# Optimization experiments

Measured on AMD Instinct MI355X. Metric: run time of the kernel, lower is better.

The kernel has to match this reference:

```python
import jax, jax.numpy as jnp
import numpy as np

N_NODES = 100000
N_EDGES = 3200000
F_IN = 16
H1 = 50
H2 = 20


def gcn_conv(x, W, b, src, dst, ew, n):
    """GCNConv with add_self_loops=True and symmetric normalization."""
    xw = x @ W  # [n, out]  (transform first: out < in traffic)
    loop = jnp.arange(n, dtype=src.dtype)
    src_f = jnp.concatenate([src, loop])
    dst_f = jnp.concatenate([dst, loop])
    ew_f = jnp.concatenate([ew, jnp.ones((n,), ew.dtype)])
    deg = jax.ops.segment_sum(ew_f, dst_f, num_segments=n)
    dinv = jnp.where(deg > 0, jax.lax.rsqrt(deg), 0.0)
    norm = dinv[src_f] * ew_f * dinv[dst_f]  # [E+n]
    agg = jax.ops.segment_sum(norm[:, None] * xw[src_f], dst_f, num_segments=n)
    return agg + b


def tgcn_cell(x, H, src, dst, ew, n, p):
    # p: dict of params for one TGCN cell
    cz = gcn_conv(x, p['wz'], p['bz'], src, dst, ew, n)
    Z = jax.nn.sigmoid(jnp.concatenate([cz, H], axis=1) @ p['lz_w'].T + p['lz_b'])
    cr = gcn_conv(x, p['wr'], p['br'], src, dst, ew, n)
    R = jax.nn.sigmoid(jnp.concatenate([cr, H], axis=1) @ p['lr_w'].T + p['lr_b'])
    ch = gcn_conv(x, p['wh'], p['bh'], src, dst, ew, n)
    Ht = jnp.tanh(jnp.concatenate([ch, H * R], axis=1) @ p['lh_w'].T + p['lh_b'])
    return Z * H + (1.0 - Z) * Ht


def _cell_params(key, fin, fout):
    ks = jax.random.split(key, 6)
    s_c = 1.0 / np.sqrt(fin)
    s_l = 1.0 / np.sqrt(2 * fout)
    names = ['z', 'r', 'h']
    p = {}
    for i, nm in enumerate(names):
        p['w' + nm] = jax.random.normal(ks[2 * i], (fin, fout), jnp.float32) * s_c
        p['b' + nm] = jnp.zeros((fout,), jnp.float32)
        p['l' + nm + '_w'] = jax.random.normal(ks[2 * i + 1], (fout, 2 * fout), jnp.float32) * s_l
        p['l' + nm + '_b'] = jnp.zeros((fout,), jnp.float32)
    return p


def setup_inputs() -> dict:
    key = jax.random.key(0)
    k = jax.random.split(key, 6)
    x = jax.random.normal(k[0], (N_NODES, F_IN), jnp.float32)
    edge_index = jax.random.randint(k[1], (2, N_EDGES), 0, N_NODES, jnp.int32)
    edge_weight = jax.random.uniform(k[2], (N_EDGES,), jnp.float32)
    p1 = _cell_params(k[3], F_IN, H1)
    p2 = _cell_params(k[4], H1, H2)
    inp = {'x': x, 'edge_index': edge_index, 'edge_weight': edge_weight}
    for nm, v in p1.items():
        inp['c1_' + nm] = v
    for nm, v in p2.items():
        inp['c2_' + nm] = v
    inp['lin_w'] = jax.random.normal(k[5], (1, H2), jnp.float32) * (1.0 / np.sqrt(H2))
    inp['lin_b'] = jnp.zeros((1,), jnp.float32)
    return inp


def reference(x, edge_index, edge_weight,
              c1_wz, c1_bz, c1_lz_w, c1_lz_b, c1_wr, c1_br, c1_lr_w, c1_lr_b,
              c1_wh, c1_bh, c1_lh_w, c1_lh_b,
              c2_wz, c2_bz, c2_lz_w, c2_lz_b, c2_wr, c2_br, c2_lr_w, c2_lr_b,
              c2_wh, c2_bh, c2_lh_w, c2_lh_b,
              lin_w, lin_b):
    n = x.shape[0]
    src, dst = edge_index[0], edge_index[1]
    p1 = dict(wz=c1_wz, bz=c1_bz, lz_w=c1_lz_w, lz_b=c1_lz_b,
              wr=c1_wr, br=c1_br, lr_w=c1_lr_w, lr_b=c1_lr_b,
              wh=c1_wh, bh=c1_bh, lh_w=c1_lh_w, lh_b=c1_lh_b)
    p2 = dict(wz=c2_wz, bz=c2_bz, lz_w=c2_lz_w, lz_b=c2_lz_b,
              wr=c2_wr, br=c2_br, lr_w=c2_lr_w, lr_b=c2_lr_b,
              wh=c2_wh, bh=c2_bh, lh_w=c2_lh_w, lh_b=c2_lh_b)
    h = tgcn_cell(x, jnp.zeros((n, H1), x.dtype), src, dst, edge_weight, n, p1)
    h = jax.nn.relu(h)  # dropout is identity in eval mode
    h = tgcn_cell(h, jnp.zeros((n, H2), x.dtype), src, dst, edge_weight, n, p2)
    h = jax.nn.relu(h)
    return h @ lin_w.T + lin_b  # [n, 1]
```

## Files before the change

### kernel.cpp

```cpp
#include <hip/hip_runtime.h>
#include <math.h>

#define N_NODES 100000
#define N_EDGES 3200000
#define F_IN 16
#define H1 50
#define H2 20
#define C1 100
#define C2 40
#define STRIDE 72
#define NB 391
#define BCAP 9216
#define EPT_A 16

__global__ void k_binA(const int* __restrict__ dst, const int* __restrict__ src,
                       const float* __restrict__ ew, int* __restrict__ gcur,
                       int2* __restrict__ ebuf) {
    __shared__ int cnt[NB];
    __shared__ int base[NB];
    int tid = threadIdx.x;
    for (int b = tid; b < NB; b += 256) cnt[b] = 0;
    __syncthreads();
    int e0 = blockIdx.x * (256 * EPT_A);
    unsigned meta[EPT_A], ewb[EPT_A];
    int bb[EPT_A], rr[EPT_A];
#pragma unroll
    for (int i = 0; i < EPT_A; ++i) {
        int e = e0 + i * 256 + tid;
        bool v = (e < N_EDGES);
        int d = v ? dst[e] : 0;
        int s = v ? src[e] : 0;
        float w = v ? ew[e] : 0.f;
        int b = d >> 8;
        int r = 0;
        if (v) r = atomicAdd(&cnt[b], 1);
        meta[i] = (unsigned)s | ((unsigned)(d & 255) << 17);
        ewb[i]  = __float_as_uint(w);
        bb[i]   = v ? b : -1;
        rr[i]   = r;
    }
    __syncthreads();
    for (int b = tid; b < NB; b += 256) {
        int c = cnt[b];
        base[b] = c ? atomicAdd(&gcur[b], c) : 0;
    }
    __syncthreads();
#pragma unroll
    for (int i = 0; i < EPT_A; ++i) {
        if (bb[i] >= 0) {
            int p = base[bb[i]] + rr[i];
            if (p < BCAP)
                ebuf[(size_t)bb[i] * BCAP + p] = make_int2((int)meta[i], (int)ewb[i]);
        }
    }
}

__global__ void k_binB(const int* __restrict__ gcur, const int2* __restrict__ ebuf,
                       int* __restrict__ cur, float* __restrict__ dinv,
                       int2* __restrict__ se) {
    __shared__ int   lcur[256];
    __shared__ float ldeg[256];
    int tid = threadIdx.x;
    int b   = blockIdx.x;
    if (tid < 256) { lcur[tid] = 0; ldeg[tid] = 0.f; }
    __syncthreads();
    int nE = min(gcur[b], BCAP);
    const int2* eb = ebuf + (size_t)b * BCAP;
    for (int i = tid; i < nE; i += 512) {
        int2 rec = eb[i];
        unsigned m = (unsigned)rec.x;
        int dlow = (int)(m >> 17);
        int s    = (int)(m & 0x1FFFFu);
        int r = atomicAdd(&lcur[dlow], 1);
        int node = (b << 8) + dlow;
        if (r < STRIDE)
            se[(size_t)node * STRIDE + r] = make_int2(s, rec.y);
        atomicAdd(&ldeg[dlow], __uint_as_float((unsigned)rec.y));
    }
    __syncthreads();
    if (tid < 256) {
        int node = (b << 8) + tid;
        if (node < N_NODES) {
            cur[node]  = node * STRIDE + min(lcur[tid], STRIDE);
            dinv[node] = rsqrtf(ldeg[tid] + 1.0f);
        }
    }
}

__global__ void k_y(const float* __restrict__ x, const float* __restrict__ dinv,
                    float* __restrict__ y) {
    int t = blockIdx.x * blockDim.x + threadIdx.x;
    int i = t >> 3, j = t & 7;
    if (i >= N_NODES) return;
    float2 v = ((const float2*)x)[(unsigned)i * 8 + j];
    float di = dinv[i];
    v.x *= di; v.y *= di;
    ((float2*)y)[(unsigned)i * 8 + j] = v;
}

__global__ void k_gather1(const int* __restrict__ cur, const int2* __restrict__ se,
                          const float* __restrict__ y, float* __restrict__ g) {
    int t = blockIdx.x * blockDim.x + threadIdx.x;
    int node = t >> 3, j = t & 7;
    if (node >= N_NODES) return;
    int beg = node * STRIDE;
    int end = min(cur[node], beg + STRIDE);
    const float2* y2 = (const float2*)y;
    float2 a0 = {0.f, 0.f}, a1 = {0.f, 0.f}, a2 = {0.f, 0.f}, a3 = {0.f, 0.f};
    int k = beg;
    for (; k + 4 <= end; k += 4) {
        int2 p0 = se[k], p1 = se[k + 1], p2 = se[k + 2], p3 = se[k + 3];
        float2 v0 = y2[(unsigned)p0.x * 8 + j];
        float2 v1 = y2[(unsigned)p1.x * 8 + j];
        float2 v2 = y2[(unsigned)p2.x * 8 + j];
        float2 v3 = y2[(unsigned)p3.x * 8 + j];
        float w0 = __int_as_float(p0.y), w1 = __int_as_float(p1.y);
        float w2 = __int_as_float(p2.y), w3 = __int_as_float(p3.y);
        a0.x = fmaf(w0, v0.x, a0.x); a0.y = fmaf(w0, v0.y, a0.y);
        a1.x = fmaf(w1, v1.x, a1.x); a1.y = fmaf(w1, v1.y, a1.y);
        a2.x = fmaf(w2, v2.x, a2.x); a2.y = fmaf(w2, v2.y, a2.y);
        a3.x = fmaf(w3, v3.x, a3.x); a3.y = fmaf(w3, v3.y, a3.y);
    }
    for (; k < end; ++k) {
        int2 p = se[k];
        float2 v = y2[(unsigned)p.x * 8 + j];
        float w = __int_as_float(p.y);
        a0.x = fmaf(w, v.x, a0.x); a0.y = fmaf(w, v.y, a0.y);
    }
    float2 r;
    r.x = (a0.x + a1.x) + (a2.x + a3.x);
    r.y = (a0.y + a1.y) + (a2.y + a3.y);
    ((float2*)g)[(unsigned)node * 8 + j] = r;
}

__global__ __launch_bounds__(256) void k_conv1_gate_xs2(
        const float* __restrict__ g, const float* __restrict__ x,
        const float* __restrict__ dinv,
        const float* __restrict__ wz, const float* __restrict__ wh,
        const float* __restrict__ cbz, const float* __restrict__ cbh,
        const float* __restrict__ lzw, const float* __restrict__ lzb,
        const float* __restrict__ lhw, const float* __restrict__ lhb,
        const float* __restrict__ w2z, const float* __restrict__ w2h,
        float* __restrict__ xs2) {
    int i = blockIdx.x * blockDim.x + threadIdx.x;
    if (i >= N_NODES) return;
    float di = dinv[i];

    float tv[F_IN];
    const float4* g4 = (const float4*)(g + (size_t)i * F_IN);
    const float4* x4 = (const float4*)(x + (size_t)i * F_IN);
#pragma unroll
    for (int q = 0; q < F_IN / 4; ++q) {
        float4 gv = g4[q], xv = x4[q];
        tv[4 * q + 0] = fmaf(di, xv.x, gv.x);
        tv[4 * q + 1] = fmaf(di, xv.y, gv.y);
        tv[4 * q + 2] = fmaf(di, xv.z, gv.z);
        tv[4 * q + 3] = fmaf(di, xv.w, gv.w);
    }

    float cz[H1], ch[H1];
#pragma unroll
    for (int j = 0; j < H1; ++j) {
        float az = 0.f, ah = 0.f;
#pragma unroll
        for (int k = 0; k < F_IN; ++k) {
            az = fmaf(tv[k], wz[k * H1 + j], az);
            ah = fmaf(tv[k], wh[k * H1 + j], ah);
        }
        cz[j] = fmaf(di, az, cbz[j]);
        ch[j] = fmaf(di, ah, cbh[j]);
    }

    float acc[C2];
#pragma unroll
    for (int c = 0; c < C2; ++c) acc[c] = 0.f;
    for (int j = 0; j < H1; ++j) {
        const float* zr = lzw + j * (2 * H1);
        const float* hrw = lhw + j * (2 * H1);
        float az = lzb[j], ah = lhb[j];
#pragma unroll
        for (int k = 0; k < H1; ++k) {
            az = fmaf(cz[k], zr[k], az);
            ah = fmaf(ch[k], hrw[k], ah);
        }
        float Z   = 1.f / (1.f + __expf(-az));
        float Ht  = 1.f - 2.f / (__expf(2.f * ah) + 1.f);
        float hrj = fmaxf((1.f - Z) * Ht, 0.f);
        const float* w2zr = w2z + j * H2;
        const float* w2hr = w2h + j * H2;
#pragma unroll
        for (int c = 0; c < H2; ++c) {
            acc[c]      = fmaf(hrj, w2zr[c], acc[c]);
            acc[H2 + c] = fmaf(hrj, w2hr[c], acc[H2 + c]);
        }
    }
    float4* o4 = (float4*)(xs2 + (size_t)i * C2);
#pragma unroll
    for (int q = 0; q < C2 / 4; ++q) {
        float4 v;
        v.x = di * acc[4 * q + 0]; v.y = di * acc[4 * q + 1];
        v.z = di * acc[4 * q + 2]; v.w = di * acc[4 * q + 3];
        o4[q] = v;
    }
}

__global__ void k_gather2(const int* __restrict__ cur, const int2* __restrict__ se,
                          const float* __restrict__ xs, float* __restrict__ acc) {
    int tid  = threadIdx.x;
    int node = blockIdx.x * 16 + tid / 20;
    unsigned j = (unsigned)(tid % 20);
    if (node >= N_NODES) return;
    int beg = node * STRIDE;
    int end = min(cur[node], beg + STRIDE);
    const float2* x2 = (const float2*)xs;
    float2 a0 = {0.f, 0.f}, a1 = {0.f, 0.f}, a2 = {0.f, 0.f}, a3 = {0.f, 0.f};
    int k = beg;
    for (; k + 4 <= end; k += 4) {
        int2 p0 = se[k], p1 = se[k + 1], p2 = se[k + 2], p3 = se[k + 3];
        float2 v0 = x2[(unsigned)p0.x * 20 + j];
        float2 v1 = x2[(unsigned)p1.x * 20 + j];
        float2 v2 = x2[(unsigned)p2.x * 20 + j];
        float2 v3 = x2[(unsigned)p3.x * 20 + j];
        float w0 = __int_as_float(p0.y), w1 = __int_as_float(p1.y);
        float w2 = __int_as_float(p2.y), w3 = __int_as_float(p3.y);
        a0.x = fmaf(w0, v0.x, a0.x); a0.y = fmaf(w0, v0.y, a0.y);
        a1.x = fmaf(w1, v1.x, a1.x); a1.y = fmaf(w1, v1.y, a1.y);
        a2.x = fmaf(w2, v2.x, a2.x); a2.y = fmaf(w2, v2.y, a2.y);
        a3.x = fmaf(w3, v3.x, a3.x); a3.y = fmaf(w3, v3.y, a3.y);
    }
    for (; k < end; ++k) {
        int2 p = se[k];
        float2 v = x2[(unsigned)p.x * 20 + j];
        float w = __int_as_float(p.y);
        a0.x = fmaf(w, v.x, a0.x); a0.y = fmaf(w, v.y, a0.y);
    }
    float2 r;
    r.x = (a0.x + a1.x) + (a2.x + a3.x);
    r.y = (a0.y + a1.y) + (a2.y + a3.y);
    ((float2*)acc)[(unsigned)node * 20 + j] = r;
}

__global__ void k_cell2_gate_out(const float* __restrict__ acc2, const float* __restrict__ xs2,
                                 const float* __restrict__ dinv,
                                 const float* __restrict__ cbz, const float* __restrict__ cbh,
                                 const float* __restrict__ lzw, const float* __restrict__ lzb,
                                 const float* __restrict__ lhw, const float* __restrict__ lhb,
                                 const float* __restrict__ linw, const float* __restrict__ linb,
                                 float* __restrict__ out) {
    __shared__ float zw[H2][H2], hw[H2][H2];
    __shared__ float zb[H2], hb[H2], lw[H2];
    __shared__ float rowbuf[64][C2 + 1];
    int tid = threadIdx.x;
    for (int t = tid; t < H2 * H2; t += 64) {
        int j = t / H2, k = t % H2;
        zw[j][k] = lzw[j * (2 * H2) + k];
        hw[j][k] = lhw[j * (2 * H2) + k];
    }
    if (tid < H2) { zb[tid] = lzb[tid]; hb[tid] = lhb[tid]; lw[tid] = linw[tid]; }
    int base = blockIdx.x * 64;
    for (int t = tid; t < 64 * C2; t += 64) {
        int il = t / C2, k = t % C2;
        size_t idx = (size_t)(base + il) * C2 + k;
        if (base + il < N_NODES) rowbuf[il][k] = acc2[idx] + xs2[idx];
    }
    __syncthreads();
    int i = base + tid;
    if (i >= N_NODES) return;
    float di = dinv[i];
    float czv[H2], chv[H2];
#pragma unroll
    for (int k = 0; k < H2; ++k) {
        czv[k] = di * rowbuf[tid][k]      + cbz[k];
        chv[k] = di * rowbuf[tid][H2 + k] + cbh[k];
    }
    float o = 0.f;
    for (int j = 0; j < H2; ++j) {
        float az = zb[j], ah = hb[j];
#pragma unroll
        for (int k = 0; k < H2; ++k) {
            az = fmaf(czv[k], zw[j][k], az);
            ah = fmaf(chv[k], hw[j][k], ah);
        }
        float Z  = 1.f / (1.f + __expf(-az));
        float Ht = 1.f - 2.f / (__expf(2.f * ah) + 1.f);
        o = fmaf(fmaxf((1.f - Z) * Ht, 0.f), lw[j], o);
    }
    out[i] = o + linb[0];
}

extern "C" void kernel_launch(void* const* d_in, const int* in_sizes, int n_in,
                              void* d_out, int out_size, void* d_ws, size_t ws_size,
                              hipStream_t stream) {
    const float* x      = (const float*)d_in[0];
    const int*   ei     = (const int*)d_in[1];
    const int*   src    = ei;
    const int*   dst    = ei + N_EDGES;
    const float* ew     = (const float*)d_in[2];
    const float* c1_wz  = (const float*)d_in[3];
    const float* c1_bz  = (const float*)d_in[4];
    const float* c1_lzw = (const float*)d_in[5];
    const float* c1_lzb = (const float*)d_in[6];
    const float* c1_wh  = (const float*)d_in[11];
    const float* c1_bh  = (const float*)d_in[12];
    const float* c1_lhw = (const float*)d_in[13];
    const float* c1_lhb = (const float*)d_in[14];
    const float* c2_wz  = (const float*)d_in[15];
    const float* c2_bz  = (const float*)d_in[16];
    const float* c2_lzw = (const float*)d_in[17];
    const float* c2_lzb = (const float*)d_in[18];
    const float* c2_wh  = (const float*)d_in[23];
    const float* c2_bh  = (const float*)d_in[24];
    const float* c2_lhw = (const float*)d_in[25];
    const float* c2_lhb = (const float*)d_in[26];
    const float* linw   = (const float*)d_in[27];
    const float* linb   = (const float*)d_in[28];
    float* out = (float*)d_out;

    int*   cur  = (int*)d_ws;
    float* dinv = (float*)(cur + N_NODES);
    int*   gcur = (int*)(dinv + N_NODES);
    int2*  se   = (int2*)(gcur + 512);
    float* xs2  = (float*)(se + (size_t)N_NODES * STRIDE);
    float* y    = xs2 + (size_t)N_NODES * C2;
    float* g    = y + (size_t)N_NODES * F_IN;
    float* acc2 = y;
    int2*  ebuf = (int2*)xs2;

    hipMemsetAsync(gcur, 0, NB * sizeof(int), stream);
    k_binA<<<(N_EDGES + 256 * EPT_A - 1) / (256 * EPT_A), 256, 0, stream>>>(
        dst, src, ew, gcur, ebuf);
    k_binB<<<NB, 512, 0, stream>>>(gcur, ebuf, cur, dinv, se);
    k_y<<<(N_NODES * 8 + 255) / 256, 256, 0, stream>>>(x, dinv, y);

    k_gather1<<<(N_NODES * 8 + 255) / 256, 256, 0, stream>>>(cur, se, y, g);
    k_conv1_gate_xs2<<<(N_NODES + 255) / 256, 256, 0, stream>>>(g, x, dinv,
        c1_wz, c1_wh, c1_bz, c1_bh, c1_lzw, c1_lzb, c1_lhw, c1_lhb,
        c2_wz, c2_wh, xs2);

    k_gather2<<<(N_NODES + 15) / 16, 320, 0, stream>>>(cur, se, xs2, acc2);
    k_cell2_gate_out<<<(N_NODES + 63) / 64, 64, 0, stream>>>(acc2, xs2, dinv,
        c2_bz, c2_bh, c2_lzw, c2_lzb, c2_lhw, c2_lhb, linw, linb, out);
}
```

Before: 447.4 us.

## Split conv1 gate kernel across two lanes per node with shuffle reduction

Measured after the change: 591.7 us. 32.3% more time.

```diff
diff --git a/kernel.cpp b/kernel.cpp
--- a/kernel.cpp
+++ b/kernel.cpp
@@ -142,7 +142,9 @@
         const float* __restrict__ lhw, const float* __restrict__ lhb,
         const float* __restrict__ w2z, const float* __restrict__ w2h,
         float* __restrict__ xs2) {
-    int i = blockIdx.x * blockDim.x + threadIdx.x;
+    int t = blockIdx.x * blockDim.x + threadIdx.x;
+    int i = t >> 1;
+    int p = t & 1;
     if (i >= N_NODES) return;
     float di = dinv[i];
 
@@ -158,45 +160,53 @@
         tv[4 * q + 3] = fmaf(di, xv.w, gv.w);
     }
 
-    float cz[H1], ch[H1];
-#pragma unroll
-    for (int j = 0; j < H1; ++j) {
+    const int kb = p * 25;
+    float cz[25], ch[25];
+#pragma unroll
+    for (int jj = 0; jj < 25; ++jj) {
+        int j = kb + jj;
         float az = 0.f, ah = 0.f;
 #pragma unroll
         for (int k = 0; k < F_IN; ++k) {
             az = fmaf(tv[k], wz[k * H1 + j], az);
             ah = fmaf(tv[k], wh[k * H1 + j], ah);
         }
-        cz[j] = fmaf(di, az, cbz[j]);
-        ch[j] = fmaf(di, ah, cbh[j]);
-    }
-
-    float acc[C2];
-#pragma unroll
-    for (int c = 0; c < C2; ++c) acc[c] = 0.f;
+        cz[jj] = fmaf(di, az, cbz[j]);
+        ch[jj] = fmaf(di, ah, cbh[j]);
+    }
+
+    float acc[H2];
+#pragma unroll
+    for (int c = 0; c < H2; ++c) acc[c] = 0.f;
+    const float* wrow_base = (p == 0) ? w2z : w2h;
     for (int j = 0; j < H1; ++j) {
-        const float* zr = lzw + j * (2 * H1);
-        const float* hrw = lhw + j * (2 * H1);
-        float az = lzb[j], ah = lhb[j];
-#pragma unroll
-        for (int k = 0; k < H1; ++k) {
-            az = fmaf(cz[k], zr[k], az);
-            ah = fmaf(ch[k], hrw[k], ah);
-        }
+        const float* zr  = lzw + j * (2 * H1) + kb;
+        const float* hrw = lhw + j * (2 * H1) + kb;
+        float az0 = 0.f, az1 = 0.f, ah0 = 0.f, ah1 = 0.f;
+#pragma unroll
+        for (int k = 0; k < 24; k += 2) {
+            az0 = fmaf(cz[k],     zr[k],      az0);
+            az1 = fmaf(cz[k + 1], zr[k + 1],  az1);
+            ah0 = fmaf(ch[k],     hrw[k],     ah0);
+            ah1 = fmaf(ch[k + 1], hrw[k + 1], ah1);
+        }
+        az0 = fmaf(cz[24], zr[24],  az0);
+        ah0 = fmaf(ch[24], hrw[24], ah0);
+        float azp = az0 + az1, ahp = ah0 + ah1;
+        azp += __shfl_xor(azp, 1, 64);
+        ahp += __shfl_xor(ahp, 1, 64);
+        float az = azp + lzb[j];
+        float ah = ahp + lhb[j];
         float Z   = 1.f / (1.f + __expf(-az));
         float Ht  = 1.f - 2.f / (__expf(2.f * ah) + 1.f);
         float hrj = fmaxf((1.f - Z) * Ht, 0.f);
-        const float* w2zr = w2z + j * H2;
-        const float* w2hr = w2h + j * H2;
-#pragma unroll
-        for (int c = 0; c < H2; ++c) {
-            acc[c]      = fmaf(hrj, w2zr[c], acc[c]);
-            acc[H2 + c] = fmaf(hrj, w2hr[c], acc[H2 + c]);
-        }
-    }
-    float4* o4 = (float4*)(xs2 + (size_t)i * C2);
-#pragma unroll
-    for (int q = 0; q < C2 / 4; ++q) {
+        const float* wrow = wrow_base + j * H2;
+#pragma unroll
+        for (int c = 0; c < H2; ++c) acc[c] = fmaf(hrj, wrow[c], acc[c]);
+    }
+    float4* o4 = (float4*)(xs2 + (size_t)i * C2 + p * H2);
+#pragma unroll
+    for (int q = 0; q < H2 / 4; ++q) {
         float4 v;
         v.x = di * acc[4 * q + 0]; v.y = di * acc[4 * q + 1];
         v.z = di * acc[4 * q + 2]; v.w = di * acc[4 * q + 3];
@@ -333,7 +343,7 @@
     k_y<<<(N_NODES * 8 + 255) / 256, 256, 0, stream>>>(x, dinv, y);
 
     k_gather1<<<(N_NODES * 8 + 255) / 256, 256, 0, stream>>>(cur, se, y, g);
-    k_conv1_gate_xs2<<<(N_NODES + 255) / 256, 256, 0, stream>>>(g, x, dinv,
+    k_conv1_gate_xs2<<<(2 * N_NODES + 255) / 256, 256, 0, stream>>>(g, x, dinv,
         c1_wz, c1_wh, c1_bz, c1_bh, c1_lzw, c1_lzb, c1_lhw, c1_lhb,
         c2_wz, c2_wh, xs2);
 
```
